# Optimization experiments

Hardware: AMD Instinct MI355X
Metric: run time of the kernel (lower is better)

## Reference

```python
import jax, jax.numpy as jnp
import numpy as np

NVFP4_VALUES = jnp.array([0.0, 0.5, 1.0, 1.5, 2.0, 3.0, 4.0, 6.0], dtype=jnp.float32)
NVFP4_MAX = 6.0


def quantize_to_nvfp4(t):
    """Fake-quantize to NVFP4 (e2m1) via nearest codebook magnitude.
    Returns (quantized_tensor, inv_scale) matching the torch reference."""
    amax = jnp.maximum(jnp.max(jnp.abs(t)), 1e-12)
    scale = NVFP4_MAX / amax                      # scalar
    scaled = jnp.clip(t.astype(jnp.float32) * scale, -NVFP4_MAX, NVFP4_MAX)
    signs = jnp.sign(scaled)
    # distance to each of the 8 e2m1 magnitudes -> nearest index
    dist = jnp.abs(jnp.abs(scaled)[..., None] - NVFP4_VALUES)  # (..., 8)
    idx = jnp.argmin(dist, axis=-1)
    quantized = signs * NVFP4_VALUES[idx]
    return quantized, 1.0 / scale


def setup_inputs() -> dict:
    key = jax.random.key(0)
    kx, kw = jax.random.split(key)
    x = jax.random.normal(kx, (512, 4096), dtype=jnp.float32)          # batch=512 (in SUPPORTED_BATCH_SIZES -> no padding)
    # kaiming-uniform-ish init for weight [out_features, in_features]
    bound = float(np.sqrt(6.0 / 4096.0))
    weight = jax.random.uniform(kw, (4096, 4096), dtype=jnp.float32,
                                minval=-bound, maxval=bound)
    return {"x": x, "weight": weight}


def reference(x, weight):
    # batch==512 is an exact supported size, so pad/unpad is identity.
    x_q, x_inv_scale = quantize_to_nvfp4(x)
    w_q, w_inv_scale = quantize_to_nvfp4(weight)
    # out[b,o] = sum_i (x_q*x_s)[b,i] * (w_q*w_s)[o,i]
    out = jnp.einsum('bi,oi->bo', x_q * x_inv_scale, w_q * w_inv_scale)
    return out.astype(x.dtype)
```

## Files before the change

### kernel.cpp

```cpp
#include <hip/hip_runtime.h>

#define M_DIM 512
#define N_DIM 4096
#define K_DIM 4096
#define KB    (K_DIM / 2)

typedef __attribute__((ext_vector_type(4))) float f32x4;
typedef __attribute__((ext_vector_type(8))) int i32x8;
typedef __attribute__((ext_vector_type(4))) int i32x4;

#define PART_X_OFF 0
#define PART_X_N   256
#define PART_W_OFF 256
#define PART_W_N   1024
#define AMAX_OFF   1280
#define XQ_BYTE_OFF 8192
#define WQ_BYTE_OFF (XQ_BYTE_OFF + M_DIM * KB)

__global__ __launch_bounds__(256) void amax_kernel(
    const float4* __restrict__ x4, const float4* __restrict__ w4,
    float* __restrict__ ws_f) {
    const int b = blockIdx.x;
    float m = 0.0f;
    if (b < PART_X_N) {
        const int n4 = M_DIM * K_DIM / 4, stride = PART_X_N * 256;
        for (int i = b * 256 + threadIdx.x; i < n4; i += stride) {
            float4 a = x4[i];
            m = fmaxf(m, fmaxf(fmaxf(fabsf(a.x), fabsf(a.y)),
                               fmaxf(fabsf(a.z), fabsf(a.w))));
        }
    } else {
        const int n4 = N_DIM * K_DIM / 4, stride = PART_W_N * 256;
        for (int i = (b - PART_X_N) * 256 + threadIdx.x; i < n4; i += stride) {
            float4 a = w4[i];
            m = fmaxf(m, fmaxf(fmaxf(fabsf(a.x), fabsf(a.y)),
                               fmaxf(fabsf(a.z), fabsf(a.w))));
        }
    }
    for (int off = 32; off > 0; off >>= 1)
        m = fmaxf(m, __shfl_down(m, off, 64));
    __shared__ float sm[4];
    if ((threadIdx.x & 63) == 0) sm[threadIdx.x >> 6] = m;
    __syncthreads();
    if (threadIdx.x == 0) {
        m = fmaxf(fmaxf(sm[0], sm[1]), fmaxf(sm[2], sm[3]));
        ws_f[(b < PART_X_N) ? (PART_X_OFF + b) : (PART_W_OFF + b - PART_X_N)] = m;
    }
}

__device__ __forceinline__ unsigned int q1n(float x, float s) {
    float a = fabsf(x) * s;
    unsigned int c;
    if      (a <= 0.25f) c = 0u;
    else if (a <= 0.75f) c = 1u;
    else if (a <= 1.25f) c = 2u;
    else if (a <= 1.75f) c = 3u;
    else if (a <= 2.5f)  c = 4u;
    else if (a <= 3.5f)  c = 5u;
    else if (a <= 5.0f)  c = 6u;
    else                 c = 7u;
    return c | ((__float_as_uint(x) >> 28) & 0x8u);
}
__device__ __forceinline__ unsigned int qpack8(float4 v0, float4 v1, float s) {
    return  q1n(v0.x, s)        | (q1n(v0.y, s) << 4)  |
           (q1n(v0.z, s) << 8)  | (q1n(v0.w, s) << 12) |
           (q1n(v1.x, s) << 16) | (q1n(v1.y, s) << 20) |
           (q1n(v1.z, s) << 24) | (q1n(v1.w, s) << 28);
}

__global__ __launch_bounds__(256) void quant_kernel(
    const float4* __restrict__ x4, const float4* __restrict__ w4,
    float* __restrict__ ws_f, unsigned char* __restrict__ ws_b) {
    const int b = blockIdx.x, t = threadIdx.x;
    const bool is_x = b < 512;
    float m = 0.0f;
    if (is_x) {
        m = ws_f[PART_X_OFF + t];
    } else {
        for (int i = t; i < PART_W_N; i += 256)
            m = fmaxf(m, ws_f[PART_W_OFF + i]);
    }
    for (int off = 32; off > 0; off >>= 1)
        m = fmaxf(m, __shfl_down(m, off, 64));
    __shared__ float sm[4];
    if ((t & 63) == 0) sm[t >> 6] = m;
    __syncthreads();
    m = fmaxf(fmaxf(sm[0], sm[1]), fmaxf(sm[2], sm[3]));
    float amax = fmaxf(m, 1e-12f);
    float s = 6.0f / amax;
    if (t == 0 && b == 0)   ws_f[AMAX_OFF + 0] = amax;
    if (t == 0 && b == 512) ws_f[AMAX_OFF + 1] = amax;

    const float4* src = is_x ? x4 : w4;
    unsigned char* dstb = ws_b + (is_x ? XQ_BYTE_OFF : WQ_BYTE_OFF);
    const int idx = (is_x ? b : b - 512) * 256 + t;
    const float4* p = src + (size_t)idx * 4;
    uint2 o;
    o.x = qpack8(p[0], p[1], s);
    o.y = qpack8(p[2], p[3], s);
    ((uint2*)dstb)[idx] = o;
}

__device__ __forceinline__ void async_copy16(const void* g, void* l) {
    __builtin_amdgcn_global_load_lds(
        (const __attribute__((address_space(1))) unsigned int*)g,
        (__attribute__((address_space(3))) unsigned int*)l, 16, 0, 0);
}

__device__ __forceinline__ i32x8 frag4(const unsigned char* rowbase,
                                       int mask, int l) {
    const i32x4 lo = *(const i32x4*)(rowbase + ((l ^ mask) * 16));
    const i32x4 z  = {0, 0, 0, 0};
    return __builtin_shufflevector(lo, z, 0, 1, 2, 3, 4, 5, 6, 7);
}

__global__ __launch_bounds__(256, 2) void gemm_kernel(
    const unsigned char* __restrict__ A, const unsigned char* __restrict__ B,
    float* __restrict__ C, const float* __restrict__ amax2) {
    __shared__ __align__(16) unsigned char As[2][64 * 256];
    __shared__ __align__(16) unsigned char Bs[2][64 * 256];

    const int bid  = blockIdx.x;
    const int bm   = (bid >> 6) * 64;
    const int bn   = ((bid & 7) * 8 + ((bid >> 3) & 7)) * 64;
    const int tid  = threadIdx.x;
    const int lane = tid & 63;
    const int wave = tid >> 6;
    const int wm   = (wave >> 1) * 32;
    const int wn   = (wave & 1) * 32;
    const int t15  = lane & 15;
    const int quad = lane >> 4;

    const float cs = (1.0f / (6.0f / fmaxf(amax2[0], 1e-12f))) *
                     (1.0f / (6.0f / fmaxf(amax2[1], 1e-12f)));

    const unsigned char* agp[4];
    const unsigned char* bgp[4];
#pragma unroll
    for (int j = 0; j < 4; j++) {
        const int c = j * 256 + tid;
        const int row = c >> 4, pcol = c & 15;
        const int gk = pcol ^ (row & 15);
        agp[j] = A + (size_t)(bm + row) * KB + gk * 16;
        bgp[j] = B + (size_t)(bn + row) * KB + gk * 16;
    }

#define STAGE(buf, kb)                                                  \
    do {                                                                \
        _Pragma("unroll")                                               \
        for (int j = 0; j < 4; j++) {                                   \
            async_copy16(agp[j] + (kb), &As[buf][(j * 256 + tid) * 16]);\
            async_copy16(bgp[j] + (kb), &Bs[buf][(j * 256 + tid) * 16]);\
        }                                                               \
    } while (0)

    f32x4 acc[2][2] = {};

    STAGE(0, 0);
#pragma unroll 2
    for (int t = 0; t < 8; ++t) {
        const int cur = t & 1;
        if (t < 7) {
            STAGE(cur ^ 1, (t + 1) * 256);
            asm volatile("s_waitcnt vmcnt(8)" ::: "memory");
        } else {
            asm volatile("s_waitcnt vmcnt(0)" ::: "memory");
        }
        __builtin_amdgcn_s_barrier();

        const unsigned char* A0 = As[cur] + (wm + t15) * 256;
        const unsigned char* A1 = A0 + 16 * 256;
        const unsigned char* B0 = Bs[cur] + (wn + t15) * 256;
        const unsigned char* B1 = B0 + 16 * 256;
#pragma unroll
        for (int s = 0; s < 4; ++s) {
            const int l0 = s * 4 + quad;
            const i32x8 af0 = frag4(A0, t15, l0);
            const i32x8 af1 = frag4(A1, t15, l0);
            const i32x8 bf0 = frag4(B0, t15, l0);
            const i32x8 bf1 = frag4(B1, t15, l0);
            acc[0][0] = __builtin_amdgcn_mfma_scale_f32_16x16x128_f8f6f4(
                af0, bf0, acc[0][0], 4, 4, 0, 0x7F7F7F7F, 0, 0x7F7F7F7F);
            acc[0][1] = __builtin_amdgcn_mfma_scale_f32_16x16x128_f8f6f4(
                af0, bf1, acc[0][1], 4, 4, 0, 0x7F7F7F7F, 0, 0x7F7F7F7F);
            acc[1][0] = __builtin_amdgcn_mfma_scale_f32_16x16x128_f8f6f4(
                af1, bf0, acc[1][0], 4, 4, 0, 0x7F7F7F7F, 0, 0x7F7F7F7F);
            acc[1][1] = __builtin_amdgcn_mfma_scale_f32_16x16x128_f8f6f4(
                af1, bf1, acc[1][1], 4, 4, 0, 0x7F7F7F7F, 0, 0x7F7F7F7F);
        }
        __builtin_amdgcn_s_barrier();
    }
#undef STAGE

#pragma unroll
    for (int i = 0; i < 2; i++)
#pragma unroll
        for (int j = 0; j < 2; j++) {
            const int m0 = bm + wm + i * 16 + quad * 4;
            const int n0 = bn + wn + j * 16 + t15;
#pragma unroll
            for (int r = 0; r < 4; r++)
                C[(size_t)(m0 + r) * N_DIM + n0] = acc[i][j][r] * cs;
        }
}

extern "C" void kernel_launch(void* const* d_in, const int* in_sizes, int n_in,
                              void* d_out, int out_size, void* d_ws, size_t ws_size,
                              hipStream_t stream) {
    const float* x = (const float*)d_in[0];
    const float* w = (const float*)d_in[1];
    float* out = (float*)d_out;

    float* ws_f = (float*)d_ws;
    unsigned char* ws_b = (unsigned char*)d_ws;
    const unsigned char* xq = ws_b + XQ_BYTE_OFF;
    const unsigned char* wq = ws_b + WQ_BYTE_OFF;

    amax_kernel<<<PART_X_N + PART_W_N, 256, 0, stream>>>(
        (const float4*)x, (const float4*)w, ws_f);
    quant_kernel<<<512 + 4096, 256, 0, stream>>>(
        (const float4*)x, (const float4*)w, ws_f, ws_b);
    gemm_kernel<<<(M_DIM / 64) * (N_DIM / 64), 256, 0, stream>>>(
        xq, wq, out, ws_f + AMAX_OFF);
}
```

Baseline: 125.5 us.

## Fuse amax, quantize and GEMM into one cooperative persistent kernel

Replaces the three separate launches (amax reduction, quantization, FP4 GEMM) with a single cooperative kernel of 512 blocks that uses grid-wide syncs between phases. Each block keeps its slice of x in registers from the amax pass so x is read only once, and W is read twice as before. This removes launch gaps and one read of x, at the cost of two grid barriers and fewer blocks for the streaming phases. If the cooperative launch fails, it falls back to the original three kernels.

```diff
diff --git a/kernel.cpp b/kernel.cpp
--- a/kernel.cpp
+++ b/kernel.cpp
@@ -1,4 +1,7 @@
 #include <hip/hip_runtime.h>
+#include <hip/hip_cooperative_groups.h>
+
+namespace cg = cooperative_groups;
 
 #define M_DIM 512
 #define N_DIM 4096
@@ -16,37 +19,6 @@
 #define AMAX_OFF   1280
 #define XQ_BYTE_OFF 8192
 #define WQ_BYTE_OFF (XQ_BYTE_OFF + M_DIM * KB)
-
-__global__ __launch_bounds__(256) void amax_kernel(
-    const float4* __restrict__ x4, const float4* __restrict__ w4,
-    float* __restrict__ ws_f) {
-    const int b = blockIdx.x;
-    float m = 0.0f;
-    if (b < PART_X_N) {
-        const int n4 = M_DIM * K_DIM / 4, stride = PART_X_N * 256;
-        for (int i = b * 256 + threadIdx.x; i < n4; i += stride) {
-            float4 a = x4[i];
-            m = fmaxf(m, fmaxf(fmaxf(fabsf(a.x), fabsf(a.y)),
-                               fmaxf(fabsf(a.z), fabsf(a.w))));
-        }
-    } else {
-        const int n4 = N_DIM * K_DIM / 4, stride = PART_W_N * 256;
-        for (int i = (b - PART_X_N) * 256 + threadIdx.x; i < n4; i += stride) {
-            float4 a = w4[i];
-            m = fmaxf(m, fmaxf(fmaxf(fabsf(a.x), fabsf(a.y)),
-                               fmaxf(fabsf(a.z), fabsf(a.w))));
-        }
-    }
-    for (int off = 32; off > 0; off >>= 1)
-        m = fmaxf(m, __shfl_down(m, off, 64));
-    __shared__ float sm[4];
-    if ((threadIdx.x & 63) == 0) sm[threadIdx.x >> 6] = m;
-    __syncthreads();
-    if (threadIdx.x == 0) {
-        m = fmaxf(fmaxf(sm[0], sm[1]), fmaxf(sm[2], sm[3]));
-        ws_f[(b < PART_X_N) ? (PART_X_OFF + b) : (PART_W_OFF + b - PART_X_N)] = m;
-    }
-}
 
 __device__ __forceinline__ unsigned int q1n(float x, float s) {
     float a = fabsf(x) * s;
@@ -68,37 +40,8 @@
            (q1n(v1.z, s) << 24) | (q1n(v1.w, s) << 28);
 }
 
-__global__ __launch_bounds__(256) void quant_kernel(
-    const float4* __restrict__ x4, const float4* __restrict__ w4,
-    float* __restrict__ ws_f, unsigned char* __restrict__ ws_b) {
-    const int b = blockIdx.x, t = threadIdx.x;
-    const bool is_x = b < 512;
-    float m = 0.0f;
-    if (is_x) {
-        m = ws_f[PART_X_OFF + t];
-    } else {
-        for (int i = t; i < PART_W_N; i += 256)
-            m = fmaxf(m, ws_f[PART_W_OFF + i]);
-    }
-    for (int off = 32; off > 0; off >>= 1)
-        m = fmaxf(m, __shfl_down(m, off, 64));
-    __shared__ float sm[4];
-    if ((t & 63) == 0) sm[t >> 6] = m;
-    __syncthreads();
-    m = fmaxf(fmaxf(sm[0], sm[1]), fmaxf(sm[2], sm[3]));
-    float amax = fmaxf(m, 1e-12f);
-    float s = 6.0f / amax;
-    if (t == 0 && b == 0)   ws_f[AMAX_OFF + 0] = amax;
-    if (t == 0 && b == 512) ws_f[AMAX_OFF + 1] = amax;
-
-    const float4* src = is_x ? x4 : w4;
-    unsigned char* dstb = ws_b + (is_x ? XQ_BYTE_OFF : WQ_BYTE_OFF);
-    const int idx = (is_x ? b : b - 512) * 256 + t;
-    const float4* p = src + (size_t)idx * 4;
-    uint2 o;
-    o.x = qpack8(p[0], p[1], s);
-    o.y = qpack8(p[2], p[3], s);
-    ((uint2*)dstb)[idx] = o;
+__device__ __forceinline__ float fmax4(float4 a) {
+    return fmaxf(fmaxf(fabsf(a.x), fabsf(a.y)), fmaxf(fabsf(a.z), fabsf(a.w)));
 }
 
 __device__ __forceinline__ void async_copy16(const void* g, void* l) {
@@ -114,31 +57,88 @@
     return __builtin_shufflevector(lo, z, 0, 1, 2, 3, 4, 5, 6, 7);
 }
 
-__global__ __launch_bounds__(256, 2) void gemm_kernel(
-    const unsigned char* __restrict__ A, const unsigned char* __restrict__ B,
-    float* __restrict__ C, const float* __restrict__ amax2) {
+__global__ __launch_bounds__(256, 2) void fused_kernel(
+    const float4* __restrict__ x4, const float4* __restrict__ w4,
+    float* __restrict__ C, float* __restrict__ ws_f,
+    unsigned char* __restrict__ ws_b) {
     __shared__ __align__(16) unsigned char As[2][64 * 256];
     __shared__ __align__(16) unsigned char Bs[2][64 * 256];
-
-    const int bid  = blockIdx.x;
-    const int bm   = (bid >> 6) * 64;
-    const int bn   = ((bid & 7) * 8 + ((bid >> 3) & 7)) * 64;
-    const int tid  = threadIdx.x;
-    const int lane = tid & 63;
-    const int wave = tid >> 6;
+    __shared__ float sm[8];
+
+    const int b = blockIdx.x;
+    const int t = threadIdx.x;
+
+    const int xidx = b * 256 + t;
+    const float4* xp = x4 + (size_t)xidx * 4;
+    const float4 xr0 = xp[0], xr1 = xp[1], xr2 = xp[2], xr3 = xp[3];
+    float mx = fmaxf(fmaxf(fmax4(xr0), fmax4(xr1)),
+                     fmaxf(fmax4(xr2), fmax4(xr3)));
+    float mw = 0.0f;
+    {
+        const int n4 = N_DIM * K_DIM / 4, stride = 512 * 256;
+        for (int i = b * 256 + t; i < n4; i += stride)
+            mw = fmaxf(mw, fmax4(w4[i]));
+    }
+    for (int off = 32; off > 0; off >>= 1) {
+        mx = fmaxf(mx, __shfl_down(mx, off, 64));
+        mw = fmaxf(mw, __shfl_down(mw, off, 64));
+    }
+    if ((t & 63) == 0) { sm[t >> 6] = mx; sm[4 + (t >> 6)] = mw; }
+    __syncthreads();
+    if (t == 0) {
+        ws_f[b]       = fmaxf(fmaxf(sm[0], sm[1]), fmaxf(sm[2], sm[3]));
+        ws_f[512 + b] = fmaxf(fmaxf(sm[4], sm[5]), fmaxf(sm[6], sm[7]));
+    }
+    cg::this_grid().sync();
+
+    float vx = fmaxf(ws_f[t], ws_f[t + 256]);
+    float vw = fmaxf(ws_f[512 + t], ws_f[768 + t]);
+    for (int off = 32; off > 0; off >>= 1) {
+        vx = fmaxf(vx, __shfl_down(vx, off, 64));
+        vw = fmaxf(vw, __shfl_down(vw, off, 64));
+    }
+    __syncthreads();
+    if ((t & 63) == 0) { sm[t >> 6] = vx; sm[4 + (t >> 6)] = vw; }
+    __syncthreads();
+    const float amax_x = fmaxf(fmaxf(fmaxf(sm[0], sm[1]), fmaxf(sm[2], sm[3])), 1e-12f);
+    const float amax_w = fmaxf(fmaxf(fmaxf(sm[4], sm[5]), fmaxf(sm[6], sm[7])), 1e-12f);
+    const float sx = 6.0f / amax_x;
+    const float sw = 6.0f / amax_w;
+    const float cs = (amax_x / 6.0f) * (amax_w / 6.0f);
+
+    {
+        uint2 o;
+        o.x = qpack8(xr0, xr1, sx);
+        o.y = qpack8(xr2, xr3, sx);
+        ((uint2*)(ws_b + XQ_BYTE_OFF))[xidx] = o;
+    }
+    for (int vb = b + 512; vb < 4608; vb += 512) {
+        const int idx = (vb - 512) * 256 + t;
+        const float4* p = w4 + (size_t)idx * 4;
+        uint2 o;
+        o.x = qpack8(p[0], p[1], sw);
+        o.y = qpack8(p[2], p[3], sw);
+        ((uint2*)(ws_b + WQ_BYTE_OFF))[idx] = o;
+    }
+    cg::this_grid().sync();
+
+    const unsigned char* A = ws_b + XQ_BYTE_OFF;
+    const unsigned char* B = ws_b + WQ_BYTE_OFF;
+
+    const int bm   = (b >> 6) * 64;
+    const int bn   = ((b & 7) * 8 + ((b >> 3) & 7)) * 64;
+    const int lane = t & 63;
+    const int wave = t >> 6;
     const int wm   = (wave >> 1) * 32;
     const int wn   = (wave & 1) * 32;
     const int t15  = lane & 15;
     const int quad = lane >> 4;
 
-    const float cs = (1.0f / (6.0f / fmaxf(amax2[0], 1e-12f))) *
-                     (1.0f / (6.0f / fmaxf(amax2[1], 1e-12f)));
-
     const unsigned char* agp[4];
     const unsigned char* bgp[4];
 #pragma unroll
     for (int j = 0; j < 4; j++) {
-        const int c = j * 256 + tid;
+        const int c = j * 256 + t;
         const int row = c >> 4, pcol = c & 15;
         const int gk = pcol ^ (row & 15);
         agp[j] = A + (size_t)(bm + row) * KB + gk * 16;
@@ -149,8 +149,8 @@
     do {                                                                \
         _Pragma("unroll")                                               \
         for (int j = 0; j < 4; j++) {                                   \
-            async_copy16(agp[j] + (kb), &As[buf][(j * 256 + tid) * 16]);\
-            async_copy16(bgp[j] + (kb), &Bs[buf][(j * 256 + tid) * 16]);\
+            async_copy16(agp[j] + (kb), &As[buf][(j * 256 + t) * 16]);  \
+            async_copy16(bgp[j] + (kb), &Bs[buf][(j * 256 + t) * 16]);  \
         }                                                               \
     } while (0)
 
@@ -158,10 +158,10 @@
 
     STAGE(0, 0);
 #pragma unroll 2
-    for (int t = 0; t < 8; ++t) {
-        const int cur = t & 1;
-        if (t < 7) {
-            STAGE(cur ^ 1, (t + 1) * 256);
+    for (int it = 0; it < 8; ++it) {
+        const int cur = it & 1;
+        if (it < 7) {
+            STAGE(cur ^ 1, (it + 1) * 256);
             asm volatile("s_waitcnt vmcnt(8)" ::: "memory");
         } else {
             asm volatile("s_waitcnt vmcnt(0)" ::: "memory");
@@ -204,6 +204,154 @@
         }
 }
 
+__global__ __launch_bounds__(256) void amax_kernel(
+    const float4* __restrict__ x4, const float4* __restrict__ w4,
+    float* __restrict__ ws_f) {
+    const int b = blockIdx.x;
+    float m = 0.0f;
+    if (b < PART_X_N) {
+        const int n4 = M_DIM * K_DIM / 4, stride = PART_X_N * 256;
+        for (int i = b * 256 + threadIdx.x; i < n4; i += stride)
+            m = fmaxf(m, fmax4(x4[i]));
+    } else {
+        const int n4 = N_DIM * K_DIM / 4, stride = PART_W_N * 256;
+        for (int i = (b - PART_X_N) * 256 + threadIdx.x; i < n4; i += stride)
+            m = fmaxf(m, fmax4(w4[i]));
+    }
+    for (int off = 32; off > 0; off >>= 1)
+        m = fmaxf(m, __shfl_down(m, off, 64));
+    __shared__ float sm[4];
+    if ((threadIdx.x & 63) == 0) sm[threadIdx.x >> 6] = m;
+    __syncthreads();
+    if (threadIdx.x == 0) {
+        m = fmaxf(fmaxf(sm[0], sm[1]), fmaxf(sm[2], sm[3]));
+        ws_f[(b < PART_X_N) ? (PART_X_OFF + b) : (PART_W_OFF + b - PART_X_N)] = m;
+    }
+}
+
+__global__ __launch_bounds__(256) void quant_kernel(
+    const float4* __restrict__ x4, const float4* __restrict__ w4,
+    float* __restrict__ ws_f, unsigned char* __restrict__ ws_b) {
+    const int b = blockIdx.x, t = threadIdx.x;
+    const bool is_x = b < 512;
+    float m = 0.0f;
+    if (is_x) {
+        m = ws_f[PART_X_OFF + t];
+    } else {
+        for (int i = t; i < PART_W_N; i += 256)
+            m = fmaxf(m, ws_f[PART_W_OFF + i]);
+    }
+    for (int off = 32; off > 0; off >>= 1)
+        m = fmaxf(m, __shfl_down(m, off, 64));
+    __shared__ float sm[4];
+    if ((t & 63) == 0) sm[t >> 6] = m;
+    __syncthreads();
+    m = fmaxf(fmaxf(sm[0], sm[1]), fmaxf(sm[2], sm[3]));
+    float amax = fmaxf(m, 1e-12f);
+    float s = 6.0f / amax;
+    if (t == 0 && b == 0)   ws_f[AMAX_OFF + 0] = amax;
+    if (t == 0 && b == 512) ws_f[AMAX_OFF + 1] = amax;
+
+    const float4* src = is_x ? x4 : w4;
+    unsigned char* dstb = ws_b + (is_x ? XQ_BYTE_OFF : WQ_BYTE_OFF);
+    const int idx = (is_x ? b : b - 512) * 256 + t;
+    const float4* p = src + (size_t)idx * 4;
+    uint2 o;
+    o.x = qpack8(p[0], p[1], s);
+    o.y = qpack8(p[2], p[3], s);
+    ((uint2*)dstb)[idx] = o;
+}
+
+__global__ __launch_bounds__(256, 2) void gemm_kernel(
+    const unsigned char* __restrict__ A, const unsigned char* __restrict__ B,
+    float* __restrict__ C, const float* __restrict__ amax2) {
+    __shared__ __align__(16) unsigned char As[2][64 * 256];
+    __shared__ __align__(16) unsigned char Bs[2][64 * 256];
+
+    const int bid  = blockIdx.x;
+    const int bm   = (bid >> 6) * 64;
+    const int bn   = ((bid & 7) * 8 + ((bid >> 3) & 7)) * 64;
+    const int tid  = threadIdx.x;
+    const int lane = tid & 63;
+    const int wave = tid >> 6;
+    const int wm   = (wave >> 1) * 32;
+    const int wn   = (wave & 1) * 32;
+    const int t15  = lane & 15;
+    const int quad = lane >> 4;
+
+    const float cs = (1.0f / (6.0f / fmaxf(amax2[0], 1e-12f))) *
+                     (1.0f / (6.0f / fmaxf(amax2[1], 1e-12f)));
+
+    const unsigned char* agp[4];
+    const unsigned char* bgp[4];
+#pragma unroll
+    for (int j = 0; j < 4; j++) {
+        const int c = j * 256 + tid;
+        const int row = c >> 4, pcol = c & 15;
+        const int gk = pcol ^ (row & 15);
+        agp[j] = A + (size_t)(bm + row) * KB + gk * 16;
+        bgp[j] = B + (size_t)(bn + row) * KB + gk * 16;
+    }
+
+#define STAGE(buf, kb)                                                  \
+    do {                                                                \
+        _Pragma("unroll")                                               \
+        for (int j = 0; j < 4; j++) {                                   \
+            async_copy16(agp[j] + (kb), &As[buf][(j * 256 + tid) * 16]);\
+            async_copy16(bgp[j] + (kb), &Bs[buf][(j * 256 + tid) * 16]);\
+        }                                                               \
+    } while (0)
+
+    f32x4 acc[2][2] = {};
+
+    STAGE(0, 0);
+#pragma unroll 2
+    for (int t = 0; t < 8; ++t) {
+        const int cur = t & 1;
+        if (t < 7) {
+            STAGE(cur ^ 1, (t + 1) * 256);
+            asm volatile("s_waitcnt vmcnt(8)" ::: "memory");
+        } else {
+            asm volatile("s_waitcnt vmcnt(0)" ::: "memory");
+        }
+        __builtin_amdgcn_s_barrier();
+
+        const unsigned char* A0 = As[cur] + (wm + t15) * 256;
+        const unsigned char* A1 = A0 + 16 * 256;
+        const unsigned char* B0 = Bs[cur] + (wn + t15) * 256;
+        const unsigned char* B1 = B0 + 16 * 256;
+#pragma unroll
+        for (int s = 0; s < 4; ++s) {
+            const int l0 = s * 4 + quad;
+            const i32x8 af0 = frag4(A0, t15, l0);
+            const i32x8 af1 = frag4(A1, t15, l0);
+            const i32x8 bf0 = frag4(B0, t15, l0);
+            const i32x8 bf1 = frag4(B1, t15, l0);
+            acc[0][0] = __builtin_amdgcn_mfma_scale_f32_16x16x128_f8f6f4(
+                af0, bf0, acc[0][0], 4, 4, 0, 0x7F7F7F7F, 0, 0x7F7F7F7F);
+            acc[0][1] = __builtin_amdgcn_mfma_scale_f32_16x16x128_f8f6f4(
+                af0, bf1, acc[0][1], 4, 4, 0, 0x7F7F7F7F, 0, 0x7F7F7F7F);
+            acc[1][0] = __builtin_amdgcn_mfma_scale_f32_16x16x128_f8f6f4(
+                af1, bf0, acc[1][0], 4, 4, 0, 0x7F7F7F7F, 0, 0x7F7F7F7F);
+            acc[1][1] = __builtin_amdgcn_mfma_scale_f32_16x16x128_f8f6f4(
+                af1, bf1, acc[1][1], 4, 4, 0, 0x7F7F7F7F, 0, 0x7F7F7F7F);
+        }
+        __builtin_amdgcn_s_barrier();
+    }
+#undef STAGE
+
+#pragma unroll
+    for (int i = 0; i < 2; i++)
+#pragma unroll
+        for (int j = 0; j < 2; j++) {
+            const int m0 = bm + wm + i * 16 + quad * 4;
+            const int n0 = bn + wn + j * 16 + t15;
+#pragma unroll
+            for (int r = 0; r < 4; r++)
+                C[(size_t)(m0 + r) * N_DIM + n0] = acc[i][j][r] * cs;
+        }
+}
+
 extern "C" void kernel_launch(void* const* d_in, const int* in_sizes, int n_in,
                               void* d_out, int out_size, void* d_ws, size_t ws_size,
                               hipStream_t stream) {
@@ -213,13 +361,25 @@
 
     float* ws_f = (float*)d_ws;
     unsigned char* ws_b = (unsigned char*)d_ws;
-    const unsigned char* xq = ws_b + XQ_BYTE_OFF;
-    const unsigned char* wq = ws_b + WQ_BYTE_OFF;
-
-    amax_kernel<<<PART_X_N + PART_W_N, 256, 0, stream>>>(
-        (const float4*)x, (const float4*)w, ws_f);
-    quant_kernel<<<512 + 4096, 256, 0, stream>>>(
-        (const float4*)x, (const float4*)w, ws_f, ws_b);
-    gemm_kernel<<<(M_DIM / 64) * (N_DIM / 64), 256, 0, stream>>>(
-        xq, wq, out, ws_f + AMAX_OFF);
-}
+
+    const float4* x4p = (const float4*)x;
+    const float4* w4p = (const float4*)w;
+    float* outp = out;
+    float* wsfp = ws_f;
+    unsigned char* wsbp = ws_b;
+    void* args[] = {(void*)&x4p, (void*)&w4p, (void*)&outp,
+                    (void*)&wsfp, (void*)&wsbp};
+
+    hipError_t err = hipLaunchCooperativeKernel(
+        (const void*)fused_kernel, dim3(512), dim3(256), args, 0, stream);
+
+    if (err != hipSuccess) {
+        (void)hipGetLastError();
+        const unsigned char* xq = wsbp + XQ_BYTE_OFF;
+        const unsigned char* wq = wsbp + WQ_BYTE_OFF;
+        amax_kernel<<<PART_X_N + PART_W_N, 256, 0, stream>>>(x4p, w4p, wsfp);
+        quant_kernel<<<512 + 4096, 256, 0, stream>>>(x4p, w4p, wsfp, wsbp);
+        gemm_kernel<<<(M_DIM / 64) * (N_DIM / 64), 256, 0, stream>>>(
+            xq, wq, out, wsfp + AMAX_OFF);
+    }
+}
```

Measured after the change: 235.8 us. 1.88x slower.
